# Performance work log

Hardware: AMD Instinct MI355X
Metric: run time of the kernel (lower is better)

## Reference

```python
import jax, jax.numpy as jnp
import numpy as np

N_NODES = 50000
N_EDGES = 800000
D = 128
H = 8
DH = D // H  # 16


def setup_inputs() -> dict:
    key = jax.random.key(0)
    ks = jax.random.split(key, 9)
    x = jax.random.normal(ks[0], (N_NODES, D), dtype=jnp.float32)
    # guarantee every node has >=1 incoming edge (avoids z == 0)
    dst_rand = jax.random.randint(ks[1], (N_EDGES - N_NODES,), 0, N_NODES, dtype=jnp.int64 if jax.config.jax_enable_x64 else jnp.int32)
    dst = jnp.concatenate([jnp.arange(N_NODES, dtype=dst_rand.dtype), dst_rand])
    src = jax.random.randint(ks[2], (N_EDGES,), 0, N_NODES, dtype=dst.dtype)
    scale = 0.05
    Wq = jax.random.normal(ks[3], (D, D), dtype=jnp.float32) * scale
    Wk = jax.random.normal(ks[4], (D, D), dtype=jnp.float32) * scale
    Wv = jax.random.normal(ks[5], (D, D), dtype=jnp.float32) * scale
    bq = jax.random.normal(ks[6], (D,), dtype=jnp.float32) * scale
    bk = jax.random.normal(ks[7], (D,), dtype=jnp.float32) * scale
    bv = jax.random.normal(ks[8], (D,), dtype=jnp.float32) * scale
    return {"x": x, "src": src, "dst": dst, "Wq": Wq, "bq": bq, "Wk": Wk, "bk": bk, "Wv": Wv, "bv": bv}


def reference(x, src, dst, Wq, bq, Wk, bk, Wv, bv):
    N = x.shape[0]
    # node projections -> [N, H, DH]
    Q = (x @ Wq + bq).reshape(N, H, DH)
    K = (x @ Wk + bk).reshape(N, H, DH)
    V = (x @ Wv + bv).reshape(N, H, DH)
    scale_const = jnp.sqrt(jnp.float32(DH))
    # per-edge score: (K[src] . Q[dst]) per head, then exp-clamp  -> [E, H]
    score = jnp.einsum('ehd,ehd->eh', K[src], Q[dst])
    score = jnp.exp(jnp.clip(score / scale_const, -5.0, 5.0))
    # scatter-sum by destination node
    wV = jax.ops.segment_sum(score[:, :, None] * V[src], dst, num_segments=N)  # [N,H,DH]
    z = jax.ops.segment_sum(score, dst, num_segments=N)  # [N,H]
    attn = (wV / z[:, :, None]).reshape(N, H * DH)
    # dropout p=0 -> identity; residual
    return x + attn
```

## Files before the change

kernel.cpp:

```cpp
#include <hip/hip_runtime.h>
#include <hip/hip_bf16.h>

#define N_NODES 50000
#define N_EDGES 800000
#define D 128
#define H 8
#define DH 16
#define SCAN_CHUNK 256
#define NCHUNK ((N_NODES + SCAN_CHUNK - 1) / SCAN_CHUNK)

typedef __attribute__((ext_vector_type(8))) short short8;
typedef __attribute__((ext_vector_type(4))) float floatx4;

__device__ __forceinline__ float bfbits2f(unsigned short u) {
    union { unsigned int i; float f; } c; c.i = ((unsigned int)u) << 16; return c.f;
}
__device__ __forceinline__ unsigned short f2bfbits(float f) {
    __hip_bfloat16 h = __float2bfloat16(f);
    return *reinterpret_cast<unsigned short*>(&h);
}

__global__ __launch_bounds__(256) void prep_w_kernel(
    const float* __restrict__ Wq, const float* __restrict__ Wk,
    const float* __restrict__ Wv, __hip_bfloat16* __restrict__ Wt,
    int* __restrict__ counts)
{
    const int i = blockIdx.x * 256 + threadIdx.x;
    if (i < N_NODES) counts[i] = 0;
    if (i >= 3 * D * D) return;
    const int p = i >> 14;
    const int r = i & (D * D - 1);
    const int col = r >> 7;
    const int k = r & (D - 1);
    const float* W = (p == 0) ? Wq : (p == 1) ? Wk : Wv;
    Wt[i] = __float2bfloat16(W[k * D + col]);
}

__global__ __launch_bounds__(256) void proj_mfma_kernel(
    const float* __restrict__ x,
    const __hip_bfloat16* __restrict__ Wt,
    const float* __restrict__ bq, const float* __restrict__ bk,
    const float* __restrict__ bv,
    unsigned short* __restrict__ Qt,
    unsigned int* __restrict__ KVi)
{
    const int m0   = blockIdx.x * 64;
    const int tid  = threadIdx.x;
    const int lane = tid & 63;
    const int wv   = tid >> 6;
    const int cb   = wv * 32;
    const int lr   = lane & 15;
    const int hi   = lane >> 4;

    __shared__ short xs[64][136];

    {
        const int row = tid >> 2;
        const int c0  = (tid & 3) * 32;
        int n = m0 + row; if (n >= N_NODES) n = N_NODES - 1;
        const float* xr = x + (size_t)n * D + c0;
        #pragma unroll
        for (int i = 0; i < 8; ++i) {
            const float4 f = *(const float4*)(xr + i * 4);
            short4 s;
            s.x = (short)f2bfbits(f.x); s.y = (short)f2bfbits(f.y);
            s.z = (short)f2bfbits(f.z); s.w = (short)f2bfbits(f.w);
            *(short4*)(&xs[row][c0 + i * 4]) = s;
        }
    }
    __syncthreads();

    floatx4 acc[3][4][2];
    #pragma unroll
    for (int p = 0; p < 3; ++p)
        #pragma unroll
        for (int rt = 0; rt < 4; ++rt)
            #pragma unroll
            for (int ct = 0; ct < 2; ++ct)
                acc[p][rt][ct] = (floatx4){0.f, 0.f, 0.f, 0.f};

    const short* Wts = (const short*)Wt;

    #pragma unroll
    for (int ks = 0; ks < 4; ++ks) {
        const int k0 = ks * 32 + hi * 8;

        short8 bfr[3][2];
        #pragma unroll
        for (int p = 0; p < 3; ++p)
            #pragma unroll
            for (int ct = 0; ct < 2; ++ct) {
                const int col = cb + ct * 16 + lr;
                bfr[p][ct] = *(const short8*)(Wts + ((size_t)(p * D + col) * D + k0));
            }

        short8 afr[4];
        #pragma unroll
        for (int rt = 0; rt < 4; ++rt)
            afr[rt] = *(const short8*)(&xs[rt * 16 + lr][k0]);

        #pragma unroll
        for (int p = 0; p < 3; ++p)
            #pragma unroll
            for (int ct = 0; ct < 2; ++ct)
                #pragma unroll
                for (int rt = 0; rt < 4; ++rt)
                    acc[p][rt][ct] = __builtin_amdgcn_mfma_f32_16x16x32_bf16(
                        afr[rt], bfr[p][ct], acc[p][rt][ct], 0, 0, 0);
    }

    #pragma unroll
    for (int ct = 0; ct < 2; ++ct) {
        const int col = cb + ct * 16 + lr;
        const float bqv = bq[col], bkv = bk[col], bvv = bv[col];
        #pragma unroll
        for (int rt = 0; rt < 4; ++rt) {
            const int node0 = m0 + rt * 16 + hi * 4;
            if (node0 < N_NODES) {
                ushort4 qs;
                qs.x = f2bfbits(acc[0][rt][ct][0] + bqv);
                qs.y = f2bfbits(acc[0][rt][ct][1] + bqv);
                qs.z = f2bfbits(acc[0][rt][ct][2] + bqv);
                qs.w = f2bfbits(acc[0][rt][ct][3] + bqv);
                *(ushort4*)(Qt + (size_t)col * N_NODES + node0) = qs;
                #pragma unroll
                for (int r = 0; r < 4; ++r) {
                    const unsigned int kk = f2bfbits(acc[1][rt][ct][r] + bkv);
                    const unsigned int vv = f2bfbits(acc[2][rt][ct][r] + bvv);
                    KVi[(size_t)(node0 + r) * 128 + col] = kk | (vv << 16);
                }
            }
        }
    }
}

__global__ __launch_bounds__(256) void hist_kernel(
    const int* __restrict__ dst, int* __restrict__ counts)
{
    const int i = blockIdx.x * blockDim.x + threadIdx.x;
    const int stride = gridDim.x * blockDim.x;
    for (int e = i; e < N_EDGES; e += stride)
        atomicAdd(&counts[dst[e]], 1);
}

__global__ __launch_bounds__(SCAN_CHUNK) void scan_a_kernel(
    const int* __restrict__ counts, int* __restrict__ row_ptr,
    int* __restrict__ blksums)
{
    __shared__ int sd[SCAN_CHUNK];
    const int tid = threadIdx.x;
    const int i   = blockIdx.x * SCAN_CHUNK + tid;
    const int v   = (i < N_NODES) ? counts[i] : 0;
    sd[tid] = v;
    __syncthreads();
    #pragma unroll
    for (int off = 1; off < SCAN_CHUNK; off <<= 1) {
        int t = (tid >= off) ? sd[tid - off] : 0;
        __syncthreads();
        sd[tid] += t;
        __syncthreads();
    }
    if (i < N_NODES) row_ptr[i] = sd[tid] - v;
    if (tid == 0) blksums[blockIdx.x] = sd[SCAN_CHUNK - 1];
}

__global__ __launch_bounds__(SCAN_CHUNK) void scan_b_kernel(int* __restrict__ blksums)
{
    __shared__ int sd[SCAN_CHUNK];
    const int tid = threadIdx.x;
    const int v = (tid < NCHUNK) ? blksums[tid] : 0;
    sd[tid] = v;
    __syncthreads();
    #pragma unroll
    for (int off = 1; off < SCAN_CHUNK; off <<= 1) {
        int t = (tid >= off) ? sd[tid - off] : 0;
        __syncthreads();
        sd[tid] += t;
        __syncthreads();
    }
    if (tid < NCHUNK) blksums[tid] = sd[tid] - v;
}

__global__ __launch_bounds__(256) void scan_c_kernel(
    int* __restrict__ row_ptr, const int* __restrict__ blksums,
    int* __restrict__ cursor)
{
    const int i = blockIdx.x * blockDim.x + threadIdx.x;
    if (i < N_NODES) {
        const int rp = row_ptr[i] + blksums[i >> 8];
        row_ptr[i] = rp;
        cursor[i] = rp;
    }
    if (i == 0) row_ptr[N_NODES] = N_EDGES;
}

__global__ __launch_bounds__(256) void scatter_kernel(
    const int* __restrict__ dst, const int* __restrict__ src,
    int* __restrict__ cursor, int* __restrict__ srcs)
{
    const int i = blockIdx.x * blockDim.x + threadIdx.x;
    const int stride = gridDim.x * blockDim.x;
    for (int e = i; e < N_EDGES; e += stride) {
        const int pos = atomicAdd(&cursor[dst[e]], 1);
        srcs[pos] = src[e];
    }
}

__global__ __launch_bounds__(256) void aggregate_kernel(
    const int* __restrict__ row_ptr, const int* __restrict__ srcs,
    const unsigned short* __restrict__ Qt, const unsigned int* __restrict__ KVi,
    const float* __restrict__ x, float* __restrict__ out)
{
    const int lane = threadIdx.x & 63;
    const int t    = (blockIdx.x * blockDim.x + threadIdx.x) >> 6;
    if (t >= N_NODES) return;

    const float q0 = bfbits2f(Qt[(size_t)(2 * lane)     * N_NODES + t]);
    const float q1 = bfbits2f(Qt[(size_t)(2 * lane + 1) * N_NODES + t]);

    int i = row_ptr[t];
    const int rp1 = row_ptr[t + 1];

    float accx = 0.f, accy = 0.f, zh = 0.f;
    const unsigned long long* KVs = (const unsigned long long*)KVi;

    for (; i + 4 <= rp1; i += 4) {
        const int s0 = srcs[i + 0];
        const int s1 = srcs[i + 1];
        const int s2 = srcs[i + 2];
        const int s3 = srcs[i + 3];
        const unsigned long long kv0 = KVs[(size_t)s0 * 64 + lane];
        const unsigned long long kv1 = KVs[(size_t)s1 * 64 + lane];
        const unsigned long long kv2 = KVs[(size_t)s2 * 64 + lane];
        const unsigned long long kv3 = KVs[(size_t)s3 * 64 + lane];

        float p0 = bfbits2f((unsigned short)kv0) * q0 + bfbits2f((unsigned short)(kv0 >> 32)) * q1;
        float p1 = bfbits2f((unsigned short)kv1) * q0 + bfbits2f((unsigned short)(kv1 >> 32)) * q1;
        float p2 = bfbits2f((unsigned short)kv2) * q0 + bfbits2f((unsigned short)(kv2 >> 32)) * q1;
        float p3 = bfbits2f((unsigned short)kv3) * q0 + bfbits2f((unsigned short)(kv3 >> 32)) * q1;

        p0 += __shfl_xor(p0, 1); p1 += __shfl_xor(p1, 1);
        p2 += __shfl_xor(p2, 1); p3 += __shfl_xor(p3, 1);
        p0 += __shfl_xor(p0, 2); p1 += __shfl_xor(p1, 2);
        p2 += __shfl_xor(p2, 2); p3 += __shfl_xor(p3, 2);
        p0 += __shfl_xor(p0, 4); p1 += __shfl_xor(p1, 4);
        p2 += __shfl_xor(p2, 4); p3 += __shfl_xor(p3, 4);

        const float w0 = __expf(fminf(fmaxf(p0 * 0.25f, -5.0f), 5.0f));
        const float w1 = __expf(fminf(fmaxf(p1 * 0.25f, -5.0f), 5.0f));
        const float w2 = __expf(fminf(fmaxf(p2 * 0.25f, -5.0f), 5.0f));
        const float w3 = __expf(fminf(fmaxf(p3 * 0.25f, -5.0f), 5.0f));

        accx += w0 * bfbits2f((unsigned short)(kv0 >> 16)) + w1 * bfbits2f((unsigned short)(kv1 >> 16))
              + w2 * bfbits2f((unsigned short)(kv2 >> 16)) + w3 * bfbits2f((unsigned short)(kv3 >> 16));
        accy += w0 * bfbits2f((unsigned short)(kv0 >> 48)) + w1 * bfbits2f((unsigned short)(kv1 >> 48))
              + w2 * bfbits2f((unsigned short)(kv2 >> 48)) + w3 * bfbits2f((unsigned short)(kv3 >> 48));
        zh   += (w0 + w1) + (w2 + w3);
    }
    for (; i < rp1; ++i) {
        const int s = srcs[i];
        const unsigned long long kv = KVs[(size_t)s * 64 + lane];
        float p = bfbits2f((unsigned short)kv) * q0 + bfbits2f((unsigned short)(kv >> 32)) * q1;
        p += __shfl_xor(p, 1);
        p += __shfl_xor(p, 2);
        p += __shfl_xor(p, 4);
        const float w = __expf(fminf(fmaxf(p * 0.25f, -5.0f), 5.0f));
        accx += w * bfbits2f((unsigned short)(kv >> 16));
        accy += w * bfbits2f((unsigned short)(kv >> 48));
        zh   += w;
    }

    const float inv = 1.0f / zh;
    const int base = t * D + 2 * lane;
    out[base + 0] = x[base + 0] + accx * inv;
    out[base + 1] = x[base + 1] + accy * inv;
}

extern "C" void kernel_launch(void* const* d_in, const int* in_sizes, int n_in,
                              void* d_out, int out_size, void* d_ws, size_t ws_size,
                              hipStream_t stream) {
    const float* x   = (const float*)d_in[0];
    const int*   src = (const int*)d_in[1];
    const int*   dst = (const int*)d_in[2];
    const float* Wq  = (const float*)d_in[3];
    const float* bq  = (const float*)d_in[4];
    const float* Wk  = (const float*)d_in[5];
    const float* bk  = (const float*)d_in[6];
    const float* Wv  = (const float*)d_in[7];
    const float* bv  = (const float*)d_in[8];

    unsigned short* Qt  = (unsigned short*)d_ws;
    unsigned int*   KVi = (unsigned int*)(Qt + (size_t)D * N_NODES);
    __hip_bfloat16* Wt  = (__hip_bfloat16*)(KVi + (size_t)N_NODES * 128);
    int* counts   = (int*)(Wt + 3 * D * D);
    int* row_ptr  = counts + 50048;
    int* cursor   = row_ptr + 50048;
    int* blksums  = cursor + 50048;
    int* srcs     = blksums + 256;

    float* out = (float*)d_out;

    prep_w_kernel<<<196, 256, 0, stream>>>(Wq, Wk, Wv, Wt, counts);

    proj_mfma_kernel<<<(N_NODES + 63) / 64, 256, 0, stream>>>(
        x, Wt, bq, bk, bv, Qt, KVi);

    hist_kernel<<<1024, 256, 0, stream>>>(dst, counts);
    scan_a_kernel<<<NCHUNK, SCAN_CHUNK, 0, stream>>>(counts, row_ptr, blksums);
    scan_b_kernel<<<1, SCAN_CHUNK, 0, stream>>>(blksums);
    scan_c_kernel<<<(N_NODES + 255) / 256, 256, 0, stream>>>(row_ptr, blksums, cursor);
    scatter_kernel<<<1024, 256, 0, stream>>>(dst, src, cursor, srcs);

    aggregate_kernel<<<(N_NODES * 64 + 255) / 256, 256, 0, stream>>>(
        row_ptr, srcs, Qt, KVi, x, out);
}
```

Baseline: 276.5 us.

## Fuse histogram into projection, single-block scan, row-major Q layout

```diff
diff --git a/kernel.cpp b/kernel.cpp
--- a/kernel.cpp
+++ b/kernel.cpp
@@ -5,9 +5,11 @@
 #define N_EDGES 800000
 #define D 128
 #define H 8
-#define DH 16
-#define SCAN_CHUNK 256
-#define NCHUNK ((N_NODES + SCAN_CHUNK - 1) / SCAN_CHUNK)
+
+#define PROJ_BLOCKS ((N_NODES + 63) / 64)
+#define HIST_BLOCKS 1024
+#define SCAN_T 1024
+#define PER_T 50
 
 typedef __attribute__((ext_vector_type(8))) short short8;
 typedef __attribute__((ext_vector_type(4))) float floatx4;
@@ -36,16 +38,26 @@
     Wt[i] = __float2bfloat16(W[k * D + col]);
 }
 
-__global__ __launch_bounds__(256) void proj_mfma_kernel(
+__global__ __launch_bounds__(256) void proj_hist_kernel(
     const float* __restrict__ x,
     const __hip_bfloat16* __restrict__ Wt,
     const float* __restrict__ bq, const float* __restrict__ bk,
     const float* __restrict__ bv,
-    unsigned short* __restrict__ Qt,
-    unsigned int* __restrict__ KVi)
-{
+    unsigned short* __restrict__ Qb,
+    unsigned int* __restrict__ KVi,
+    const int* __restrict__ dst, int* __restrict__ counts)
+{
+    const int tid = threadIdx.x;
+
+    if (blockIdx.x >= PROJ_BLOCKS) {
+        const int i = (blockIdx.x - PROJ_BLOCKS) * 256 + tid;
+        const int stride = HIST_BLOCKS * 256;
+        for (int e = i; e < N_EDGES; e += stride)
+            atomicAdd(&counts[dst[e]], 1);
+        return;
+    }
+
     const int m0   = blockIdx.x * 64;
-    const int tid  = threadIdx.x;
     const int lane = tid & 63;
     const int wv   = tid >> 6;
     const int cb   = wv * 32;
@@ -112,17 +124,11 @@
     #pragma unroll
     for (int ct = 0; ct < 2; ++ct) {
         const int col = cb + ct * 16 + lr;
-        const float bqv = bq[col], bkv = bk[col], bvv = bv[col];
+        const float bkv = bk[col], bvv = bv[col];
         #pragma unroll
         for (int rt = 0; rt < 4; ++rt) {
             const int node0 = m0 + rt * 16 + hi * 4;
             if (node0 < N_NODES) {
-                ushort4 qs;
-                qs.x = f2bfbits(acc[0][rt][ct][0] + bqv);
-                qs.y = f2bfbits(acc[0][rt][ct][1] + bqv);
-                qs.z = f2bfbits(acc[0][rt][ct][2] + bqv);
-                qs.w = f2bfbits(acc[0][rt][ct][3] + bqv);
-                *(ushort4*)(Qt + (size_t)col * N_NODES + node0) = qs;
                 #pragma unroll
                 for (int r = 0; r < 4; ++r) {
                     const unsigned int kk = f2bfbits(acc[1][rt][ct][r] + bkv);
@@ -132,66 +138,74 @@
             }
         }
     }
-}
-
-__global__ __launch_bounds__(256) void hist_kernel(
-    const int* __restrict__ dst, int* __restrict__ counts)
-{
-    const int i = blockIdx.x * blockDim.x + threadIdx.x;
-    const int stride = gridDim.x * blockDim.x;
-    for (int e = i; e < N_EDGES; e += stride)
-        atomicAdd(&counts[dst[e]], 1);
-}
-
-__global__ __launch_bounds__(SCAN_CHUNK) void scan_a_kernel(
+
+    __syncthreads();
+    #pragma unroll
+    for (int ct = 0; ct < 2; ++ct) {
+        const int col = cb + ct * 16 + lr;
+        const float bqv = bq[col];
+        #pragma unroll
+        for (int rt = 0; rt < 4; ++rt) {
+            const int nloc = rt * 16 + hi * 4;
+            #pragma unroll
+            for (int r = 0; r < 4; ++r)
+                xs[nloc + r][col] = (short)f2bfbits(acc[0][rt][ct][r] + bqv);
+        }
+    }
+    __syncthreads();
+    {
+        const int row = tid >> 2;
+        const int c0  = (tid & 3) * 32;
+        const int n   = m0 + row;
+        if (n < N_NODES) {
+            int4* dstp = (int4*)(Qb + (size_t)n * D + c0);
+            const int4* srcp = (const int4*)(&xs[row][c0]);
+            #pragma unroll
+            for (int i = 0; i < 4; ++i) dstp[i] = srcp[i];
+        }
+    }
+}
+
+__global__ __launch_bounds__(SCAN_T) void scan_kernel(
     const int* __restrict__ counts, int* __restrict__ row_ptr,
-    int* __restrict__ blksums)
-{
-    __shared__ int sd[SCAN_CHUNK];
-    const int tid = threadIdx.x;
-    const int i   = blockIdx.x * SCAN_CHUNK + tid;
-    const int v   = (i < N_NODES) ? counts[i] : 0;
-    sd[tid] = v;
-    __syncthreads();
-    #pragma unroll
-    for (int off = 1; off < SCAN_CHUNK; off <<= 1) {
-        int t = (tid >= off) ? sd[tid - off] : 0;
-        __syncthreads();
-        sd[tid] += t;
-        __syncthreads();
-    }
-    if (i < N_NODES) row_ptr[i] = sd[tid] - v;
-    if (tid == 0) blksums[blockIdx.x] = sd[SCAN_CHUNK - 1];
-}
-
-__global__ __launch_bounds__(SCAN_CHUNK) void scan_b_kernel(int* __restrict__ blksums)
-{
-    __shared__ int sd[SCAN_CHUNK];
-    const int tid = threadIdx.x;
-    const int v = (tid < NCHUNK) ? blksums[tid] : 0;
-    sd[tid] = v;
-    __syncthreads();
-    #pragma unroll
-    for (int off = 1; off < SCAN_CHUNK; off <<= 1) {
-        int t = (tid >= off) ? sd[tid - off] : 0;
-        __syncthreads();
-        sd[tid] += t;
-        __syncthreads();
-    }
-    if (tid < NCHUNK) blksums[tid] = sd[tid] - v;
-}
-
-__global__ __launch_bounds__(256) void scan_c_kernel(
-    int* __restrict__ row_ptr, const int* __restrict__ blksums,
     int* __restrict__ cursor)
 {
-    const int i = blockIdx.x * blockDim.x + threadIdx.x;
-    if (i < N_NODES) {
-        const int rp = row_ptr[i] + blksums[i >> 8];
-        row_ptr[i] = rp;
-        cursor[i] = rp;
-    }
-    if (i == 0) row_ptr[N_NODES] = N_EDGES;
+    __shared__ int wsum[16];
+    const int tid  = threadIdx.x;
+    const int base = tid * PER_T;
+
+    int tot = 0;
+    if (tid < 1000) {
+        #pragma unroll 10
+        for (int j = 0; j < PER_T; ++j) tot += counts[base + j];
+    }
+
+    int incl = tot;
+    #pragma unroll
+    for (int off = 1; off < 64; off <<= 1) {
+        const int v = __shfl_up(incl, off);
+        if ((tid & 63) >= off) incl += v;
+    }
+    if ((tid & 63) == 63) wsum[tid >> 6] = incl;
+    __syncthreads();
+    if (tid == 0) {
+        int run = 0;
+        #pragma unroll
+        for (int w = 0; w < 16; ++w) { const int v = wsum[w]; wsum[w] = run; run += v; }
+    }
+    __syncthreads();
+
+    if (tid < 1000) {
+        int run = (incl - tot) + wsum[tid >> 6];
+        #pragma unroll 10
+        for (int j = 0; j < PER_T; ++j) {
+            const int c = counts[base + j];
+            row_ptr[base + j] = run;
+            cursor[base + j]  = run;
+            run += c;
+        }
+    }
+    if (tid == 0) row_ptr[N_NODES] = N_EDGES;
 }
 
 __global__ __launch_bounds__(256) void scatter_kernel(
@@ -208,15 +222,16 @@
 
 __global__ __launch_bounds__(256) void aggregate_kernel(
     const int* __restrict__ row_ptr, const int* __restrict__ srcs,
-    const unsigned short* __restrict__ Qt, const unsigned int* __restrict__ KVi,
+    const unsigned short* __restrict__ Qb, const unsigned int* __restrict__ KVi,
     const float* __restrict__ x, float* __restrict__ out)
 {
     const int lane = threadIdx.x & 63;
     const int t    = (blockIdx.x * blockDim.x + threadIdx.x) >> 6;
     if (t >= N_NODES) return;
 
-    const float q0 = bfbits2f(Qt[(size_t)(2 * lane)     * N_NODES + t]);
-    const float q1 = bfbits2f(Qt[(size_t)(2 * lane + 1) * N_NODES + t]);
+    const unsigned int qbits = *(const unsigned int*)(Qb + (size_t)t * D + 2 * lane);
+    const float q0 = bfbits2f((unsigned short)(qbits & 0xffff));
+    const float q1 = bfbits2f((unsigned short)(qbits >> 16));
 
     int i = row_ptr[t];
     const int rp1 = row_ptr[t + 1];
@@ -289,28 +304,25 @@
     const float* Wv  = (const float*)d_in[7];
     const float* bv  = (const float*)d_in[8];
 
-    unsigned short* Qt  = (unsigned short*)d_ws;
-    unsigned int*   KVi = (unsigned int*)(Qt + (size_t)D * N_NODES);
+    unsigned short* Qb  = (unsigned short*)d_ws;
+    unsigned int*   KVi = (unsigned int*)(Qb + (size_t)N_NODES * D);
     __hip_bfloat16* Wt  = (__hip_bfloat16*)(KVi + (size_t)N_NODES * 128);
     int* counts   = (int*)(Wt + 3 * D * D);
     int* row_ptr  = counts + 50048;
     int* cursor   = row_ptr + 50048;
-    int* blksums  = cursor + 50048;
-    int* srcs     = blksums + 256;
+    int* srcs     = cursor + 50048;
 
     float* out = (float*)d_out;
 
     prep_w_kernel<<<196, 256, 0, stream>>>(Wq, Wk, Wv, Wt, counts);
 
-    proj_mfma_kernel<<<(N_NODES + 63) / 64, 256, 0, stream>>>(
-        x, Wt, bq, bk, bv, Qt, KVi);
-
-    hist_kernel<<<1024, 256, 0, stream>>>(dst, counts);
-    scan_a_kernel<<<NCHUNK, SCAN_CHUNK, 0, stream>>>(counts, row_ptr, blksums);
-    scan_b_kernel<<<1, SCAN_CHUNK, 0, stream>>>(blksums);
-    scan_c_kernel<<<(N_NODES + 255) / 256, 256, 0, stream>>>(row_ptr, blksums, cursor);
+    proj_hist_kernel<<<PROJ_BLOCKS + HIST_BLOCKS, 256, 0, stream>>>(
+        x, Wt, bq, bk, bv, Qb, KVi, dst, counts);
+
+    scan_kernel<<<1, SCAN_T, 0, stream>>>(counts, row_ptr, cursor);
+
     scatter_kernel<<<1024, 256, 0, stream>>>(dst, src, cursor, srcs);
 
     aggregate_kernel<<<(N_NODES * 64 + 255) / 256, 256, 0, stream>>>(
-        row_ptr, srcs, Qt, KVi, x, out);
-}
+        row_ptr, srcs, Qb, KVi, x, out);
+}
```

Result: no change. 275.6 us (-0.3%).
